# Kernel tuning notes

Hardware: AMD Instinct MI355X
Metric: run time of the kernel (lower is better)

## Reference

```python
import jax, jax.numpy as jnp
import numpy as np

B, N, H, E = 4, 256, 128, 16
EIN = 2 * H + 1 + E  # edge MLP input dim
LN_EPS = 1e-6  # flax nnx.LayerNorm default epsilon


def layer_norm(x, scale, bias):
    m = jnp.mean(x, axis=-1, keepdims=True)
    v = jnp.var(x, axis=-1, keepdims=True)
    return (x - m) * jax.lax.rsqrt(v + LN_EPS) * scale + bias


def mlp2(x, W1, b1, s, sb, W2, b2):
    # Linear -> LayerNorm -> ReLU -> Linear (dropout deterministic)
    h = jax.nn.relu(layer_norm(x @ W1 + b1, s, sb))
    return h @ W2 + b2


def setup_inputs() -> dict:
    key = jax.random.key(0)
    ks = jax.random.split(key, 24)

    def lin(k, fi, fo):
        k1, k2 = jax.random.split(k)
        W = jax.random.normal(k1, (fi, fo), jnp.float32) / np.sqrt(fi)
        b = jnp.zeros((fo,), jnp.float32)
        return W, b

    We1, be1 = lin(ks[0], EIN, H)
    We2, be2 = lin(ks[1], H, H)
    Wa, ba = lin(ks[2], EIN, 1)
    Wn1, bn1 = lin(ks[3], 2 * H, H)
    Wn2, bn2 = lin(ks[4], H, H)
    Wc1, bc1 = lin(ks[5], H, H)
    Wc2, bc2 = lin(ks[6], H, 1)

    return {
        "node_features": jax.random.normal(ks[7], (B, N, H), jnp.float32),
        "coordinates": jax.random.normal(ks[8], (B, N, 3), jnp.float32),
        "edge_features": jax.random.normal(ks[9], (B, N, N, E), jnp.float32),
        "mask": jnp.ones((B, N), jnp.float32),
        "We1": We1, "be1": be1,
        "ln_e_s": jnp.ones((H,), jnp.float32), "ln_e_b": jnp.zeros((H,), jnp.float32),
        "We2": We2, "be2": be2,
        "Wa": Wa, "ba": ba,
        "Wn1": Wn1, "bn1": bn1,
        "ln_n_s": jnp.ones((H,), jnp.float32), "ln_n_b": jnp.zeros((H,), jnp.float32),
        "Wn2": Wn2, "bn2": bn2,
        "Wc1": Wc1, "bc1": bc1,
        "ln_c_s": jnp.ones((H,), jnp.float32), "ln_c_b": jnp.zeros((H,), jnp.float32),
        "Wc2": Wc2, "bc2": bc2,
        "edge_index": jax.random.randint(ks[10], (B, N, N), 0, 2, jnp.int32),
    }


def reference(node_features, coordinates, edge_features, mask,
              We1, be1, ln_e_s, ln_e_b, We2, be2,
              Wa, ba,
              Wn1, bn1, ln_n_s, ln_n_b, Wn2, bn2,
              Wc1, bc1, ln_c_s, ln_c_b, Wc2, bc2,
              edge_index):
    b, n, h = node_features.shape
    rel_pos = coordinates[:, :, None, :] - coordinates[:, None, :, :]  # [B,N,N,3]
    d2 = jnp.sum(rel_pos ** 2, axis=-1, keepdims=True)                 # [B,N,N,1]

    node_i = jnp.broadcast_to(node_features[:, :, None, :], (b, n, n, h))
    node_j = jnp.broadcast_to(node_features[:, None, :, :], (b, n, n, h))
    edge_inputs = jnp.concatenate([node_i, node_j, d2, edge_features], axis=-1)  # [B,N,N,EIN]

    edge_messages = mlp2(edge_inputs, We1, be1, ln_e_s, ln_e_b, We2, be2)  # [B,N,N,H]
    new_edge_features = edge_messages

    att = jax.nn.sigmoid(edge_inputs @ Wa + ba)  # [B,N,N,1]
    adj = edge_index[..., None].astype(edge_messages.dtype)  # [B,N,N,1]
    msg_mask = (mask[:, :, None] * mask[:, None, :])[..., None]

    edge_messages = edge_messages * att * adj * msg_mask
    node_messages = jnp.sum(edge_messages, axis=2)  # [B,N,H]

    node_inputs = jnp.concatenate([node_features, node_messages], axis=-1)
    new_node_features = mlp2(node_inputs, Wn1, bn1, ln_n_s, ln_n_b, Wn2, bn2)

    coord_messages = mlp2(node_messages, Wc1, bc1, ln_c_s, ln_c_b, Wc2, bc2)  # [B,N,1]

    norm = jnp.sqrt(d2 + 1e-8)
    normalized_rel_pos = rel_pos / norm
    coord_update_dir = jnp.sum(normalized_rel_pos * att * adj, axis=2)  # [B,N,3]
    coord_updates = coord_update_dir * coord_messages * mask[:, :, None]
    new_coordinates = coordinates + coord_updates

    new_node_features = node_features + new_node_features  # residual
    return (new_node_features, new_coordinates, new_edge_features)
```

## Files before the change

### kernel.cpp

```cpp
#include <hip/hip_runtime.h>
#include <hip/hip_bf16.h>


typedef unsigned short ushort_t;
typedef __attribute__((ext_vector_type(8))) short short8;
typedef __attribute__((ext_vector_type(4))) float f32x4;

__device__ __forceinline__ ushort_t f2bf(float f) {
  unsigned int x = __builtin_bit_cast(unsigned int, f);
  x += 0x7fffu + ((x >> 16) & 1u);
  return (ushort_t)(x >> 16);
}

__global__ void k_sent777(float* out0) { out0[threadIdx.x] = 777.f; }

__global__ __launch_bounds__(128)
void k_pre(const float* nf, const float* We1, const float* be1,
           const float* Wa, float* pre_i, float* pre_j, float* api, float* apj) {
  int r = blockIdx.x, t = threadIdx.x;
  __shared__ float nfv[128];
  __shared__ float red[4];
  nfv[t] = nf[(size_t)r * 128 + t];
  __syncthreads();
  float s1 = be1[t], s2 = 0.f;
  for (int c = 0; c < 128; ++c) {
    float x = nfv[c];
    s1 += x * We1[c * 128 + t];
    s2 += x * We1[(128 + c) * 128 + t];
  }
  pre_i[(size_t)r * 128 + t] = s1;
  pre_j[(size_t)r * 128 + t] = s2;
  float t1 = nfv[t] * Wa[t];
  float t2 = nfv[t] * Wa[128 + t];
#pragma unroll
  for (int o = 32; o > 0; o >>= 1) { t1 += __shfl_down(t1, o); t2 += __shfl_down(t2, o); }
  if ((t & 63) == 0) { red[(t >> 6) * 2] = t1; red[(t >> 6) * 2 + 1] = t2; }
  __syncthreads();
  if (t == 0) { api[r] = red[0] + red[2]; apj[r] = red[1] + red[3]; }
}

__global__ __launch_bounds__(256)
void k_pack(const float* We2, ushort_t* bpack) {
  int t = blockIdx.x * 256 + threadIdx.x;
  if (t >= 2048) return;
  int ks = t >> 9, mt = (t >> 6) & 7, l = t & 63;
  int kb = ks * 32 + (l >> 4) * 8, col = mt * 16 + (l & 15);
#pragma unroll
  for (int e = 0; e < 8; ++e) bpack[t * 8 + e] = f2bf(We2[(kb + e) * 128 + col]);
}

__global__ __launch_bounds__(512, 4)
void k_edge(const float* co, const float* efo, const float* mk,
            const float* We1, const float* be2, const float* Wa, const float* ba,
            const float* lnes, const float* lneb, const int* eidx,
            const float* pre_i, const float* pre_j, const float* api, const float* apj,
            const ushort_t* bpack, float* oute, float* nm2, float* cd2) {
  __shared__ __align__(16) ushort_t h1s[128 * 136];
  __shared__ float wef[17 * 128];
  __shared__ float lns[128], lnb[128];
  __shared__ float attw[128];
  __shared__ float lnS[512], lnSS[512];
  __shared__ float nmp[8][128];
  __shared__ float cred[2][3];

  const int bx = blockIdx.x;
  const int r = bx >> 1, half = bx & 1;
  const int b = r >> 8;
  const int t = threadIdx.x;
  const int lane = t & 63, w = t >> 6;

  for (int q = t; q < 17 * 128; q += 512) {
    int e = q >> 7, c = q & 127;
    int row = (e < 16) ? (257 + e) : 256;
    wef[q] = We1[row * 128 + c];
  }
  if (t < 128) { lns[t] = lnes[t]; }
  else if (t < 256) { lnb[t - 128] = lneb[t - 128]; }
  __syncthreads();

  const int jr = t & 127, ch = t >> 7;
  const int j = half * 128 + jr;
  const int gj = b * 256 + j;

  float dx = co[r * 3 + 0] - co[gj * 3 + 0];
  float dy = co[r * 3 + 1] - co[gj * 3 + 1];
  float dz = co[r * 3 + 2] - co[gj * 3 + 2];
  float d2 = dx * dx + dy * dy + dz * dz;

  float efv[17];
  {
    const float* efp = efo + ((size_t)r * 256 + j) * 16;
    f32x4 e0 = *reinterpret_cast<const f32x4*>(efp);
    f32x4 e1 = *reinterpret_cast<const f32x4*>(efp + 4);
    f32x4 e2 = *reinterpret_cast<const f32x4*>(efp + 8);
    f32x4 e3 = *reinterpret_cast<const f32x4*>(efp + 12);
#pragma unroll
    for (int x = 0; x < 4; ++x) {
      efv[x] = e0[x]; efv[4 + x] = e1[x]; efv[8 + x] = e2[x]; efv[12 + x] = e3[x];
    }
  }
  efv[16] = d2;

  if (ch == 0) {
    float a = api[r] + apj[gj] + ba[0] + d2 * Wa[256];
#pragma unroll
    for (int e = 0; e < 16; ++e) a += efv[e] * Wa[257 + e];
    float att = 1.f / (1.f + __expf(-a));
    float aw = att * (float)eidx[(size_t)r * 256 + j];
    attw[jr] = aw * mk[r] * mk[gj];
    float invn = rsqrtf(d2 + 1e-8f);
    float c0 = dx * invn * aw, c1 = dy * invn * aw, c2 = dz * invn * aw;
#pragma unroll
    for (int o = 32; o > 0; o >>= 1) {
      c0 += __shfl_down(c0, o); c1 += __shfl_down(c1, o); c2 += __shfl_down(c2, o);
    }
    if (lane == 0) { cred[w][0] = c0; cred[w][1] = c1; cred[w][2] = c2; }
  }

  const int cbase = ch * 32;
  const f32x4* pi4 = reinterpret_cast<const f32x4*>(pre_i + (size_t)r * 128 + cbase);
  const f32x4* pj4 = reinterpret_cast<const f32x4*>(pre_j + (size_t)gj * 128 + cbase);
  const f32x4* wef4 = reinterpret_cast<const f32x4*>(wef);
  float h[32];
  float s = 0.f, ss = 0.f;
#pragma unroll
  for (int c4 = 0; c4 < 8; ++c4) {
    f32x4 v = pi4[c4] + pj4[c4];
#pragma unroll
    for (int e = 0; e < 17; ++e) v += efv[e] * wef4[e * 32 + (cbase >> 2) + c4];
#pragma unroll
    for (int x = 0; x < 4; ++x) { h[c4 * 4 + x] = v[x]; s += v[x]; ss += v[x] * v[x]; }
  }
  lnS[t] = s; lnSS[t] = ss;
  __syncthreads();
  float st  = lnS[jr] + lnS[jr + 128] + lnS[jr + 256] + lnS[jr + 384];
  float sst = lnSS[jr] + lnSS[jr + 128] + lnSS[jr + 256] + lnSS[jr + 384];
  float mean = st * (1.f / 128.f);
  float var = fmaxf(sst * (1.f / 128.f) - mean * mean, 0.f);
  float rsv = rsqrtf(var + 1e-6f);
  ushort_t* hrow = h1s + jr * 136 + cbase;
#pragma unroll
  for (int q8 = 0; q8 < 4; ++q8) {
    short8 pk;
#pragma unroll
    for (int x = 0; x < 8; ++x) {
      int c = q8 * 8 + x;
      float gv = (h[c] - mean) * rsv * lns[cbase + c] + lnb[cbase + c];
      pk[x] = (short)f2bf(fmaxf(gv, 0.f));
    }
    *reinterpret_cast<short8*>(hrow + q8 * 8) = pk;
  }
  __syncthreads();

  if (t == 0) {
#pragma unroll
    for (int d = 0; d < 3; ++d)
      cd2[(size_t)(half * 1024 + r) * 3 + d] = cred[0][d] + cred[1][d];
  }

  f32x4 acc[8];
#pragma unroll
  for (int mt = 0; mt < 8; ++mt) acc[mt] = (f32x4){0.f, 0.f, 0.f, 0.f};

  const short* h1p = reinterpret_cast<const short*>(h1s);
  const int nrow = w * 16 + (lane & 15);
#pragma unroll
  for (int ks = 0; ks < 4; ++ks) {
    short8 hfr = *reinterpret_cast<const short8*>(
        h1p + nrow * 136 + ks * 32 + ((lane >> 4) * 8));
#pragma unroll
    for (int mt = 0; mt < 8; ++mt) {
      short8 afr = *reinterpret_cast<const short8*>(bpack + (((ks * 8 + mt) * 64 + lane) * 8));
      acc[mt] = __builtin_amdgcn_mfma_f32_16x16x32_bf16(afr, hfr, acc[mt], 0, 0, 0);
    }
  }

  const size_t obase = ((size_t)r * 256 + half * 128) * 128;
  const float wgt = attw[nrow];
  const int mq = (lane >> 4) * 4;
  float pm[8][4];
#pragma unroll
  for (int mt = 0; mt < 8; ++mt) {
    f32x4 b4 = *reinterpret_cast<const f32x4*>(be2 + mt * 16 + mq);
    f32x4 val = acc[mt] + b4;
    *reinterpret_cast<f32x4*>(oute + obase + (size_t)nrow * 128 + mt * 16 + mq) = val;
#pragma unroll
    for (int x = 0; x < 4; ++x) pm[mt][x] = val[x] * wgt;
  }
#pragma unroll
  for (int mt = 0; mt < 8; ++mt)
#pragma unroll
    for (int x = 0; x < 4; ++x) {
      float v = pm[mt][x];
      v += __shfl_xor(v, 1); v += __shfl_xor(v, 2);
      v += __shfl_xor(v, 4); v += __shfl_xor(v, 8);
      pm[mt][x] = v;
    }
  if ((lane & 15) == 0) {
#pragma unroll
    for (int mt = 0; mt < 8; ++mt)
#pragma unroll
      for (int x = 0; x < 4; ++x) nmp[w][mt * 16 + mq + x] = pm[mt][x];
  }
  __syncthreads();
  if (t < 128) {
    float acc8 = nmp[0][t] + nmp[1][t] + nmp[2][t] + nmp[3][t]
               + nmp[4][t] + nmp[5][t] + nmp[6][t] + nmp[7][t];
    nm2[(size_t)(half * 1024 + r) * 128 + t] = acc8;
  }
}

__device__ __forceinline__ float bsum128(float v, float* red, int t) {
#pragma unroll
  for (int o = 32; o > 0; o >>= 1) v += __shfl_down(v, o);
  __syncthreads();
  if ((t & 63) == 0) red[t >> 6] = v;
  __syncthreads();
  return red[0] + red[1];
}

__global__ __launch_bounds__(128)
void k_node(const float* nf, const float* co, const float* mk,
            const float* Wn1, const float* bn1, const float* lnns, const float* lnnb,
            const float* Wn2, const float* bn2,
            const float* Wc1, const float* bc1, const float* lncs, const float* lncb,
            const float* Wc2, const float* bc2,
            const float* nm2, const float* cd2,
            float* out0, float* out1) {
  int r = blockIdx.x, t = threadIdx.x;
  __shared__ float nin[256];
  __shared__ float hf[128];
  __shared__ float red[2];
  float nfv = nf[(size_t)r * 128 + t];
  float nmv = nm2[(size_t)r * 128 + t] + nm2[(size_t)(1024 + r) * 128 + t];
  nin[t] = nfv; nin[128 + t] = nmv;
  __syncthreads();
  float s1 = bn1[t];
  for (int c = 0; c < 256; ++c) s1 += nin[c] * Wn1[c * 128 + t];
  float mean = bsum128(s1, red, t) * (1.f / 128.f);
  float var = fmaxf(bsum128(s1 * s1, red, t) * (1.f / 128.f) - mean * mean, 0.f);
  float hv = (s1 - mean) * rsqrtf(var + 1e-6f) * lnns[t] + lnnb[t];
  hv = fmaxf(hv, 0.f);
  hf[t] = hv;
  __syncthreads();
  float o1 = bn2[t] + nfv;
  for (int c = 0; c < 128; ++c) o1 += hf[c] * Wn2[c * 128 + t];
  out0[(size_t)r * 128 + t] = o1;
  float g = bc1[t];
  for (int c = 0; c < 128; ++c) g += nin[128 + c] * Wc1[c * 128 + t];
  float gm = bsum128(g, red, t) * (1.f / 128.f);
  float gv = fmaxf(bsum128(g * g, red, t) * (1.f / 128.f) - gm * gm, 0.f);
  float gh = fmaxf((g - gm) * rsqrtf(gv + 1e-6f) * lncs[t] + lncb[t], 0.f);
  float cm = bsum128(gh * Wc2[t], red, t) + bc2[0];
  if (t < 3) {
    float cd = cd2[(size_t)r * 3 + t] + cd2[(size_t)(1024 + r) * 3 + t];
    float nc = co[(size_t)r * 3 + t] + cd * cm * mk[r];
    out1[(size_t)r * 3 + t] = nc;
  }
}

extern "C" void kernel_launch(void* const* d_in, const int* in_sizes, int n_in,
                              void* d_out, int out_size, void* d_ws, size_t ws_size,
                              hipStream_t stream) {
  const float* nf   = (const float*)d_in[0];
  const float* co   = (const float*)d_in[1];
  const float* efo  = (const float*)d_in[2];
  const float* mk   = (const float*)d_in[3];
  const float* We1  = (const float*)d_in[4];
  const float* be1  = (const float*)d_in[5];
  const float* lnes = (const float*)d_in[6];
  const float* lneb = (const float*)d_in[7];
  const float* We2  = (const float*)d_in[8];
  const float* be2  = (const float*)d_in[9];
  const float* Wa   = (const float*)d_in[10];
  const float* ba   = (const float*)d_in[11];
  const float* Wn1  = (const float*)d_in[12];
  const float* bn1  = (const float*)d_in[13];
  const float* lnns = (const float*)d_in[14];
  const float* lnnb = (const float*)d_in[15];
  const float* Wn2  = (const float*)d_in[16];
  const float* bn2  = (const float*)d_in[17];
  const float* Wc1  = (const float*)d_in[18];
  const float* bc1  = (const float*)d_in[19];
  const float* lncs = (const float*)d_in[20];
  const float* lncb = (const float*)d_in[21];
  const float* Wc2  = (const float*)d_in[22];
  const float* bc2  = (const float*)d_in[23];
  const int* eidx   = (const int*)d_in[24];

  float* out0 = (float*)d_out;
  float* out1 = out0 + 131072;
  float* oute = out1 + 3072;

  const size_t need = (size_t)(131072 + 131072 + 1024 + 1024 + 262144 + 6144) * 4 + 16384 * 2;
  if (ws_size < need) {
    k_sent777<<<1, 128, 0, stream>>>(out0);
    return;
  }
  float* ws    = (float*)d_ws;
  float* pre_i = ws;
  float* pre_j = pre_i + 131072;
  float* api   = pre_j + 131072;
  float* apj   = api + 1024;
  float* nm2   = apj + 1024;
  float* cd2   = nm2 + 262144;
  ushort_t* bpack = (ushort_t*)(cd2 + 6144);

  k_pre<<<1024, 128, 0, stream>>>(nf, We1, be1, Wa, pre_i, pre_j, api, apj);
  k_pack<<<8, 256, 0, stream>>>(We2, bpack);
  k_edge<<<2048, 512, 0, stream>>>(co, efo, mk, We1, be2, Wa, ba, lnes, lneb, eidx,
                                   pre_i, pre_j, api, apj, bpack, oute, nm2, cd2);
  k_node<<<1024, 128, 0, stream>>>(nf, co, mk, Wn1, bn1, lnns, lnnb, Wn2, bn2,
                                   Wc1, bc1, lncs, lncb, Wc2, bc2, nm2, cd2, out0, out1);
}
```

Baseline: 114.3 us.

## Compute first edge-MLP layer's edge-feature projection with bf16 MFMA

Replaces the per-thread scalar FMA loop over 17 edge inputs with a bf16 MFMA 16x16x32 call. The A operand (edge features plus d2, zero-padded) is staged in LDS and the We1 fragment is held in registers. LayerNorm statistics are now computed from a bf16-rounded copy of the hidden row written to LDS, and the old partial-sum arrays and weight LDS tables are removed. Occupancy hint is lowered from 4 to 2 blocks per CU. This adds bf16 rounding of the edge features and pre-LN values, which may hurt accuracy, plus extra LDS passes and uncoalesced per-element h1s writes.

```diff
diff --git a/kernel.cpp b/kernel.cpp
--- a/kernel.cpp
+++ b/kernel.cpp
@@ -10,6 +10,10 @@
   unsigned int x = __builtin_bit_cast(unsigned int, f);
   x += 0x7fffu + ((x >> 16) & 1u);
   return (ushort_t)(x >> 16);
+}
+__device__ __forceinline__ float bf2f(ushort_t u) {
+  unsigned int x = ((unsigned int)u) << 16;
+  return __builtin_bit_cast(float, x);
 }
 
 __global__ void k_sent777(float* out0) { out0[threadIdx.x] = 777.f; }
@@ -49,17 +53,16 @@
   for (int e = 0; e < 8; ++e) bpack[t * 8 + e] = f2bf(We2[(kb + e) * 128 + col]);
 }
 
-__global__ __launch_bounds__(512, 4)
+__global__ __launch_bounds__(512, 2)
 void k_edge(const float* co, const float* efo, const float* mk,
             const float* We1, const float* be2, const float* Wa, const float* ba,
             const float* lnes, const float* lneb, const int* eidx,
             const float* pre_i, const float* pre_j, const float* api, const float* apj,
             const ushort_t* bpack, float* oute, float* nm2, float* cd2) {
+  __shared__ __align__(16) ushort_t A_lds[8 * 64 * 8];
   __shared__ __align__(16) ushort_t h1s[128 * 136];
-  __shared__ float wef[17 * 128];
-  __shared__ float lns[128], lnb[128];
+  __shared__ float2 mrsv[128];
   __shared__ float attw[128];
-  __shared__ float lnS[512], lnSS[512];
   __shared__ float nmp[8][128];
   __shared__ float cred[2][3];
 
@@ -68,27 +71,47 @@
   const int b = r >> 8;
   const int t = threadIdx.x;
   const int lane = t & 63, w = t >> 6;
-
-  for (int q = t; q < 17 * 128; q += 512) {
-    int e = q >> 7, c = q & 127;
-    int row = (e < 16) ? (257 + e) : 256;
-    wef[q] = We1[row * 128 + c];
-  }
-  if (t < 128) { lns[t] = lnes[t]; }
-  else if (t < 256) { lnb[t - 128] = lneb[t - 128]; }
-  __syncthreads();
-
-  const int jr = t & 127, ch = t >> 7;
-  const int j = half * 128 + jr;
-  const int gj = b * 256 + j;
-
-  float dx = co[r * 3 + 0] - co[gj * 3 + 0];
-  float dy = co[r * 3 + 1] - co[gj * 3 + 1];
-  float dz = co[r * 3 + 2] - co[gj * 3 + 2];
-  float d2 = dx * dx + dy * dy + dz * dz;
-
-  float efv[17];
+  const int s4 = lane >> 4;
+  const int chan = w * 16 + (lane & 15);
+  const int gbase = b * 256 + half * 128;
+
+  short8 wfrag;
+#pragma unroll
+  for (int e = 0; e < 8; ++e) {
+    int k = s4 * 8 + e;
+    float wv = 0.f;
+    if (k < 16) wv = We1[(257 + k) * 128 + chan];
+    else if (k == 16) wv = We1[256 * 128 + chan];
+    wfrag[e] = (short)f2bf(wv);
+  }
+  const float preIc = pre_i[(size_t)r * 128 + chan];
+  const float lnsc = lnes[chan], lnbc = lneb[chan];
+
   {
+    const int mt = t >> 6, l = t & 63, sl = l >> 4, row = mt * 16 + (l & 15);
+    short8* dst = reinterpret_cast<short8*>(A_lds + ((size_t)(mt * 64 + l)) * 8);
+    if (sl < 2) {
+      const float* efp = efo + ((size_t)(r * 256 + half * 128 + row)) * 16 + sl * 8;
+      f32x4 e0 = *reinterpret_cast<const f32x4*>(efp);
+      f32x4 e1 = *reinterpret_cast<const f32x4*>(efp + 4);
+      short8 pk;
+#pragma unroll
+      for (int x = 0; x < 4; ++x) { pk[x] = (short)f2bf(e0[x]); pk[4 + x] = (short)f2bf(e1[x]); }
+      *dst = pk;
+    } else if (sl == 3) {
+      *dst = (short8){0, 0, 0, 0, 0, 0, 0, 0};
+    }
+  }
+
+  if (t < 128) {
+    const int j = half * 128 + t;
+    const int gj = b * 256 + j;
+    float dx = co[r * 3 + 0] - co[gj * 3 + 0];
+    float dy = co[r * 3 + 1] - co[gj * 3 + 1];
+    float dz = co[r * 3 + 2] - co[gj * 3 + 2];
+    float d2 = dx * dx + dy * dy + dz * dz;
+
+    float a = api[r] + apj[gj] + ba[0] + d2 * Wa[256];
     const float* efp = efo + ((size_t)r * 256 + j) * 16;
     f32x4 e0 = *reinterpret_cast<const f32x4*>(efp);
     f32x4 e1 = *reinterpret_cast<const f32x4*>(efp + 4);
@@ -96,18 +119,17 @@
     f32x4 e3 = *reinterpret_cast<const f32x4*>(efp + 12);
 #pragma unroll
     for (int x = 0; x < 4; ++x) {
-      efv[x] = e0[x]; efv[4 + x] = e1[x]; efv[8 + x] = e2[x]; efv[12 + x] = e3[x];
-    }
-  }
-  efv[16] = d2;
-
-  if (ch == 0) {
-    float a = api[r] + apj[gj] + ba[0] + d2 * Wa[256];
-#pragma unroll
-    for (int e = 0; e < 16; ++e) a += efv[e] * Wa[257 + e];
+      a += e0[x] * Wa[257 + x] + e1[x] * Wa[261 + x]
+         + e2[x] * Wa[265 + x] + e3[x] * Wa[269 + x];
+    }
     float att = 1.f / (1.f + __expf(-a));
     float aw = att * (float)eidx[(size_t)r * 256 + j];
-    attw[jr] = aw * mk[r] * mk[gj];
+    attw[t] = aw * mk[r] * mk[gj];
+
+    short8 dz8 = (short8){0, 0, 0, 0, 0, 0, 0, 0};
+    dz8[0] = (short)f2bf(d2);
+    *reinterpret_cast<short8*>(A_lds + ((size_t)((t >> 4) * 64 + 32 + (t & 15))) * 8) = dz8;
+
     float invn = rsqrtf(d2 + 1e-8f);
     float c0 = dx * invn * aw, c1 = dy * invn * aw, c2 = dz * invn * aw;
 #pragma unroll
@@ -116,39 +138,54 @@
     }
     if (lane == 0) { cred[w][0] = c0; cred[w][1] = c1; cred[w][2] = c2; }
   }
-
-  const int cbase = ch * 32;
-  const f32x4* pi4 = reinterpret_cast<const f32x4*>(pre_i + (size_t)r * 128 + cbase);
-  const f32x4* pj4 = reinterpret_cast<const f32x4*>(pre_j + (size_t)gj * 128 + cbase);
-  const f32x4* wef4 = reinterpret_cast<const f32x4*>(wef);
-  float h[32];
-  float s = 0.f, ss = 0.f;
-#pragma unroll
-  for (int c4 = 0; c4 < 8; ++c4) {
-    f32x4 v = pi4[c4] + pj4[c4];
-#pragma unroll
-    for (int e = 0; e < 17; ++e) v += efv[e] * wef4[e * 32 + (cbase >> 2) + c4];
-#pragma unroll
-    for (int x = 0; x < 4; ++x) { h[c4 * 4 + x] = v[x]; s += v[x]; ss += v[x] * v[x]; }
-  }
-  lnS[t] = s; lnSS[t] = ss;
-  __syncthreads();
-  float st  = lnS[jr] + lnS[jr + 128] + lnS[jr + 256] + lnS[jr + 384];
-  float sst = lnSS[jr] + lnSS[jr + 128] + lnSS[jr + 256] + lnSS[jr + 384];
-  float mean = st * (1.f / 128.f);
-  float var = fmaxf(sst * (1.f / 128.f) - mean * mean, 0.f);
-  float rsv = rsqrtf(var + 1e-6f);
-  ushort_t* hrow = h1s + jr * 136 + cbase;
-#pragma unroll
-  for (int q8 = 0; q8 < 4; ++q8) {
-    short8 pk;
-#pragma unroll
-    for (int x = 0; x < 8; ++x) {
-      int c = q8 * 8 + x;
-      float gv = (h[c] - mean) * rsv * lns[cbase + c] + lnb[cbase + c];
-      pk[x] = (short)f2bf(fmaxf(gv, 0.f));
-    }
-    *reinterpret_cast<short8*>(hrow + q8 * 8) = pk;
+  __syncthreads();
+
+  f32x4 acc1[8];
+#pragma unroll
+  for (int mt = 0; mt < 8; ++mt) {
+    short8 afr = *reinterpret_cast<const short8*>(A_lds + ((size_t)(mt * 64 + lane)) * 8);
+    acc1[mt] = __builtin_amdgcn_mfma_f32_16x16x32_bf16(
+        afr, wfrag, (f32x4){0.f, 0.f, 0.f, 0.f}, 0, 0, 0);
+  }
+#pragma unroll
+  for (int mt = 0; mt < 8; ++mt) {
+#pragma unroll
+    for (int reg = 0; reg < 4; ++reg) {
+      int row = mt * 16 + s4 * 4 + reg;
+      float v = acc1[mt][reg] + preIc + pre_j[((size_t)(gbase + row)) * 128 + chan];
+      acc1[mt][reg] = v;
+      h1s[row * 136 + chan] = f2bf(v);
+    }
+  }
+  __syncthreads();
+
+  if (t < 128) {
+    const short8* hr8 = reinterpret_cast<const short8*>(h1s + t * 136);
+    float sum = 0.f, ss = 0.f;
+#pragma unroll
+    for (int q = 0; q < 16; ++q) {
+      short8 pk = hr8[q];
+#pragma unroll
+      for (int x = 0; x < 8; ++x) {
+        float f = bf2f((ushort_t)pk[x]);
+        sum += f; ss += f * f;
+      }
+    }
+    float mean = sum * (1.f / 128.f);
+    float var = fmaxf(ss * (1.f / 128.f) - mean * mean, 0.f);
+    mrsv[t] = make_float2(mean, rsqrtf(var + 1e-6f));
+  }
+  __syncthreads();
+
+#pragma unroll
+  for (int mt = 0; mt < 8; ++mt) {
+#pragma unroll
+    for (int reg = 0; reg < 4; ++reg) {
+      int row = mt * 16 + s4 * 4 + reg;
+      float2 mr = mrsv[row];
+      float gv = (acc1[mt][reg] - mr.x) * mr.y * lnsc + lnbc;
+      h1s[row * 136 + chan] = f2bf(fmaxf(gv, 0.f));
+    }
   }
   __syncthreads();
 
@@ -167,7 +204,7 @@
 #pragma unroll
   for (int ks = 0; ks < 4; ++ks) {
     short8 hfr = *reinterpret_cast<const short8*>(
-        h1p + nrow * 136 + ks * 32 + ((lane >> 4) * 8));
+        h1p + nrow * 136 + ks * 32 + (s4 * 8));
 #pragma unroll
     for (int mt = 0; mt < 8; ++mt) {
       short8 afr = *reinterpret_cast<const short8*>(bpack + (((ks * 8 + mt) * 64 + lane) * 8));
@@ -177,7 +214,7 @@
 
   const size_t obase = ((size_t)r * 256 + half * 128) * 128;
   const float wgt = attw[nrow];
-  const int mq = (lane >> 4) * 4;
+  const int mq = s4 * 4;
   float pm[8][4];
 #pragma unroll
   for (int mt = 0; mt < 8; ++mt) {
```

Result: faster. 101.1 us (-11.5%).

## Compute edge first-layer features with MFMA and per-wave LayerNorm reductions

Applied to the files above, without the earlier changes.

The fp32 FMA loop over the 17 edge-feature and distance inputs is replaced by a bf16 MFMA against a prepacked We1 slice, and each wave now owns 16 edge rows in the MFMA layout. LayerNorm statistics are reduced with cross-lane shuffles instead of shared-memory staging, which removes the weight and LN-parameter shared buffers and one barrier. Attention and coordinate reductions are done per wave with xor shuffles. Launch bounds are raised to 8 waves/SIMD occupancy hint. The cost is bf16 rounding of edge features and d2 in the first layer, which could hurt accuracy.

```diff
diff --git a/kernel.cpp b/kernel.cpp
--- a/kernel.cpp
+++ b/kernel.cpp
@@ -4,6 +4,7 @@
 
 typedef unsigned short ushort_t;
 typedef __attribute__((ext_vector_type(8))) short short8;
+typedef __attribute__((ext_vector_type(4))) short short4_t;
 typedef __attribute__((ext_vector_type(4))) float f32x4;
 
 __device__ __forceinline__ ushort_t f2bf(float f) {
@@ -40,46 +41,47 @@
 }
 
 __global__ __launch_bounds__(256)
-void k_pack(const float* We2, ushort_t* bpack) {
+void k_pack(const float* We2, const float* We1, ushort_t* bpack, ushort_t* wpack) {
   int t = blockIdx.x * 256 + threadIdx.x;
-  if (t >= 2048) return;
-  int ks = t >> 9, mt = (t >> 6) & 7, l = t & 63;
-  int kb = ks * 32 + (l >> 4) * 8, col = mt * 16 + (l & 15);
-#pragma unroll
-  for (int e = 0; e < 8; ++e) bpack[t * 8 + e] = f2bf(We2[(kb + e) * 128 + col]);
-}
-
-__global__ __launch_bounds__(512, 4)
+  if (t < 2048) {
+    int ks = t >> 9, mt = (t >> 6) & 7, l = t & 63;
+    int kb = ks * 32 + (l >> 4) * 8, col = mt * 16 + (l & 15);
+#pragma unroll
+    for (int e = 0; e < 8; ++e) bpack[t * 8 + e] = f2bf(We2[(kb + e) * 128 + col]);
+  } else if (t < 2560) {
+    int q = t - 2048;
+    int mt = q >> 6, l = q & 63;
+    int chan = mt * 16 + (l & 15), kb = (l >> 4) * 8;
+#pragma unroll
+    for (int e = 0; e < 8; ++e) {
+      int k = kb + e;
+      float wv = 0.f;
+      if (k < 16) wv = We1[(257 + k) * 128 + chan];
+      else if (k == 16) wv = We1[256 * 128 + chan];
+      wpack[q * 8 + e] = f2bf(wv);
+    }
+  }
+}
+
+__global__ __launch_bounds__(512, 8)
 void k_edge(const float* co, const float* efo, const float* mk,
-            const float* We1, const float* be2, const float* Wa, const float* ba,
+            const float* be2, const float* Wa, const float* ba,
             const float* lnes, const float* lneb, const int* eidx,
             const float* pre_i, const float* pre_j, const float* api, const float* apj,
-            const ushort_t* bpack, float* oute, float* nm2, float* cd2) {
+            const ushort_t* bpack, const ushort_t* wpack,
+            float* oute, float* nm2, float* cd2) {
   __shared__ __align__(16) ushort_t h1s[128 * 136];
-  __shared__ float wef[17 * 128];
-  __shared__ float lns[128], lnb[128];
-  __shared__ float attw[128];
-  __shared__ float lnS[512], lnSS[512];
   __shared__ float nmp[8][128];
-  __shared__ float cred[2][3];
+  __shared__ float cred[8][3];
 
   const int bx = blockIdx.x;
   const int r = bx >> 1, half = bx & 1;
   const int b = r >> 8;
   const int t = threadIdx.x;
   const int lane = t & 63, w = t >> 6;
-
-  for (int q = t; q < 17 * 128; q += 512) {
-    int e = q >> 7, c = q & 127;
-    int row = (e < 16) ? (257 + e) : 256;
-    wef[q] = We1[row * 128 + c];
-  }
-  if (t < 128) { lns[t] = lnes[t]; }
-  else if (t < 256) { lnb[t - 128] = lneb[t - 128]; }
-  __syncthreads();
-
-  const int jr = t & 127, ch = t >> 7;
-  const int j = half * 128 + jr;
+  const int s4 = lane >> 4, li = lane & 15;
+  const int row = w * 16 + li;
+  const int j = half * 128 + row;
   const int gj = b * 256 + j;
 
   float dx = co[r * 3 + 0] - co[gj * 3 + 0];
@@ -87,75 +89,87 @@
   float dz = co[r * 3 + 2] - co[gj * 3 + 2];
   float d2 = dx * dx + dy * dy + dz * dz;
 
-  float efv[17];
+  short8 bfr = (short8){0, 0, 0, 0, 0, 0, 0, 0};
+  float dot = 0.f;
+  if (s4 < 2) {
+    const float* efp = efo + ((size_t)r * 256 + j) * 16 + s4 * 8;
+    f32x4 a0 = *reinterpret_cast<const f32x4*>(efp);
+    f32x4 a1 = *reinterpret_cast<const f32x4*>(efp + 4);
+#pragma unroll
+    for (int x = 0; x < 4; ++x) { bfr[x] = (short)f2bf(a0[x]); bfr[4 + x] = (short)f2bf(a1[x]); }
+    const float* wap = Wa + 257 + s4 * 8;
+#pragma unroll
+    for (int x = 0; x < 4; ++x) dot += a0[x] * wap[x] + a1[x] * wap[4 + x];
+  } else if (s4 == 2) {
+    bfr[0] = (short)f2bf(d2);
+    dot = api[r] + apj[gj] + ba[0] + d2 * Wa[256];
+  }
+  dot += __shfl_xor(dot, 16);
+  dot += __shfl_xor(dot, 32);
+  float att = 1.f / (1.f + __expf(-dot));
+  float aw = att * (float)eidx[(size_t)r * 256 + j];
+  const float wgt = aw * mk[r] * mk[gj];
+
   {
-    const float* efp = efo + ((size_t)r * 256 + j) * 16;
-    f32x4 e0 = *reinterpret_cast<const f32x4*>(efp);
-    f32x4 e1 = *reinterpret_cast<const f32x4*>(efp + 4);
-    f32x4 e2 = *reinterpret_cast<const f32x4*>(efp + 8);
-    f32x4 e3 = *reinterpret_cast<const f32x4*>(efp + 12);
+    float invn = rsqrtf(d2 + 1e-8f);
+    float c0 = (s4 == 0) ? dx * invn * aw : 0.f;
+    float c1 = (s4 == 0) ? dy * invn * aw : 0.f;
+    float c2 = (s4 == 0) ? dz * invn * aw : 0.f;
+#pragma unroll
+    for (int o = 1; o < 64; o <<= 1) {
+      c0 += __shfl_xor(c0, o); c1 += __shfl_xor(c1, o); c2 += __shfl_xor(c2, o);
+    }
+    if (lane == 0) { cred[w][0] = c0; cred[w][1] = c1; cred[w][2] = c2; }
+  }
+
+  f32x4 acc1[8];
+#pragma unroll
+  for (int mt = 0; mt < 8; ++mt) {
+    short8 wfr = *reinterpret_cast<const short8*>(wpack + ((size_t)(mt * 64 + lane)) * 8);
+    acc1[mt] = __builtin_amdgcn_mfma_f32_16x16x32_bf16(
+        wfr, bfr, (f32x4){0.f, 0.f, 0.f, 0.f}, 0, 0, 0);
+  }
+
+  const float* pir = pre_i + (size_t)r * 128;
+  const float* pjr = pre_j + (size_t)gj * 128;
+  float s = 0.f, ss = 0.f;
+#pragma unroll
+  for (int mt = 0; mt < 8; ++mt) {
+    const int c0i = mt * 16 + s4 * 4;
+    f32x4 pj = *reinterpret_cast<const f32x4*>(pjr + c0i);
+    f32x4 pi = *reinterpret_cast<const f32x4*>(pir + c0i);
+    acc1[mt] += pi + pj;
+#pragma unroll
+    for (int x = 0; x < 4; ++x) { s += acc1[mt][x]; ss += acc1[mt][x] * acc1[mt][x]; }
+  }
+  s += __shfl_xor(s, 16);  s += __shfl_xor(s, 32);
+  ss += __shfl_xor(ss, 16); ss += __shfl_xor(ss, 32);
+  const float mean = s * (1.f / 128.f);
+  const float var = fmaxf(ss * (1.f / 128.f) - mean * mean, 0.f);
+  const float rsv = rsqrtf(var + 1e-6f);
+
+  ushort_t* hrow = h1s + row * 136;
+#pragma unroll
+  for (int mt = 0; mt < 8; ++mt) {
+    const int c0i = mt * 16 + s4 * 4;
+    f32x4 ln4 = *reinterpret_cast<const f32x4*>(lnes + c0i);
+    f32x4 lb4 = *reinterpret_cast<const f32x4*>(lneb + c0i);
+    short4_t pk;
 #pragma unroll
     for (int x = 0; x < 4; ++x) {
-      efv[x] = e0[x]; efv[4 + x] = e1[x]; efv[8 + x] = e2[x]; efv[12 + x] = e3[x];
-    }
-  }
-  efv[16] = d2;
-
-  if (ch == 0) {
-    float a = api[r] + apj[gj] + ba[0] + d2 * Wa[256];
-#pragma unroll
-    for (int e = 0; e < 16; ++e) a += efv[e] * Wa[257 + e];
-    float att = 1.f / (1.f + __expf(-a));
-    float aw = att * (float)eidx[(size_t)r * 256 + j];
-    attw[jr] = aw * mk[r] * mk[gj];
-    float invn = rsqrtf(d2 + 1e-8f);
-    float c0 = dx * invn * aw, c1 = dy * invn * aw, c2 = dz * invn * aw;
-#pragma unroll
-    for (int o = 32; o > 0; o >>= 1) {
-      c0 += __shfl_down(c0, o); c1 += __shfl_down(c1, o); c2 += __shfl_down(c2, o);
-    }
-    if (lane == 0) { cred[w][0] = c0; cred[w][1] = c1; cred[w][2] = c2; }
-  }
-
-  const int cbase = ch * 32;
-  const f32x4* pi4 = reinterpret_cast<const f32x4*>(pre_i + (size_t)r * 128 + cbase);
-  const f32x4* pj4 = reinterpret_cast<const f32x4*>(pre_j + (size_t)gj * 128 + cbase);
-  const f32x4* wef4 = reinterpret_cast<const f32x4*>(wef);
-  float h[32];
-  float s = 0.f, ss = 0.f;
-#pragma unroll
-  for (int c4 = 0; c4 < 8; ++c4) {
-    f32x4 v = pi4[c4] + pj4[c4];
-#pragma unroll
-    for (int e = 0; e < 17; ++e) v += efv[e] * wef4[e * 32 + (cbase >> 2) + c4];
-#pragma unroll
-    for (int x = 0; x < 4; ++x) { h[c4 * 4 + x] = v[x]; s += v[x]; ss += v[x] * v[x]; }
-  }
-  lnS[t] = s; lnSS[t] = ss;
-  __syncthreads();
-  float st  = lnS[jr] + lnS[jr + 128] + lnS[jr + 256] + lnS[jr + 384];
-  float sst = lnSS[jr] + lnSS[jr + 128] + lnSS[jr + 256] + lnSS[jr + 384];
-  float mean = st * (1.f / 128.f);
-  float var = fmaxf(sst * (1.f / 128.f) - mean * mean, 0.f);
-  float rsv = rsqrtf(var + 1e-6f);
-  ushort_t* hrow = h1s + jr * 136 + cbase;
-#pragma unroll
-  for (int q8 = 0; q8 < 4; ++q8) {
-    short8 pk;
-#pragma unroll
-    for (int x = 0; x < 8; ++x) {
-      int c = q8 * 8 + x;
-      float gv = (h[c] - mean) * rsv * lns[cbase + c] + lnb[cbase + c];
+      float gv = (acc1[mt][x] - mean) * rsv * ln4[x] + lb4[x];
       pk[x] = (short)f2bf(fmaxf(gv, 0.f));
     }
-    *reinterpret_cast<short8*>(hrow + q8 * 8) = pk;
+    *reinterpret_cast<short4_t*>(hrow + c0i) = pk;
   }
   __syncthreads();
 
   if (t == 0) {
 #pragma unroll
     for (int d = 0; d < 3; ++d)
-      cd2[(size_t)(half * 1024 + r) * 3 + d] = cred[0][d] + cred[1][d];
+      cd2[(size_t)(half * 1024 + r) * 3 + d] =
+          ((cred[0][d] + cred[1][d]) + (cred[2][d] + cred[3][d]))
+        + ((cred[4][d] + cred[5][d]) + (cred[6][d] + cred[7][d]));
   }
 
   f32x4 acc[8];
@@ -163,11 +177,9 @@
   for (int mt = 0; mt < 8; ++mt) acc[mt] = (f32x4){0.f, 0.f, 0.f, 0.f};
 
   const short* h1p = reinterpret_cast<const short*>(h1s);
-  const int nrow = w * 16 + (lane & 15);
 #pragma unroll
   for (int ks = 0; ks < 4; ++ks) {
-    short8 hfr = *reinterpret_cast<const short8*>(
-        h1p + nrow * 136 + ks * 32 + ((lane >> 4) * 8));
+    short8 hfr = *reinterpret_cast<const short8*>(h1p + row * 136 + ks * 32 + s4 * 8);
 #pragma unroll
     for (int mt = 0; mt < 8; ++mt) {
       short8 afr = *reinterpret_cast<const short8*>(bpack + (((ks * 8 + mt) * 64 + lane) * 8));
@@ -176,14 +188,13 @@
   }
 
   const size_t obase = ((size_t)r * 256 + half * 128) * 128;
-  const float wgt = attw[nrow];
-  const int mq = (lane >> 4) * 4;
+  const int mq = s4 * 4;
   float pm[8][4];
 #pragma unroll
   for (int mt = 0; mt < 8; ++mt) {
     f32x4 b4 = *reinterpret_cast<const f32x4*>(be2 + mt * 16 + mq);
     f32x4 val = acc[mt] + b4;
-    *reinterpret_cast<f32x4*>(oute + obase + (size_t)nrow * 128 + mt * 16 + mq) = val;
+    *reinterpret_cast<f32x4*>(oute + obase + (size_t)row * 128 + mt * 16 + mq) = val;
 #pragma unroll
     for (int x = 0; x < 4; ++x) pm[mt][x] = val[x] * wgt;
   }
@@ -196,7 +207,7 @@
       v += __shfl_xor(v, 4); v += __shfl_xor(v, 8);
       pm[mt][x] = v;
     }
-  if ((lane & 15) == 0) {
+  if (li == 0) {
 #pragma unroll
     for (int mt = 0; mt < 8; ++mt)
 #pragma unroll
@@ -204,8 +215,8 @@
   }
   __syncthreads();
   if (t < 128) {
-    float acc8 = nmp[0][t] + nmp[1][t] + nmp[2][t] + nmp[3][t]
-               + nmp[4][t] + nmp[5][t] + nmp[6][t] + nmp[7][t];
+    float acc8 = ((nmp[0][t] + nmp[1][t]) + (nmp[2][t] + nmp[3][t]))
+               + ((nmp[4][t] + nmp[5][t]) + (nmp[6][t] + nmp[7][t]));
     nm2[(size_t)(half * 1024 + r) * 128 + t] = acc8;
   }
 }
@@ -292,7 +303,8 @@
   float* out1 = out0 + 131072;
   float* oute = out1 + 3072;
 
-  const size_t need = (size_t)(131072 + 131072 + 1024 + 1024 + 262144 + 6144) * 4 + 16384 * 2;
+  const size_t need = (size_t)(131072 + 131072 + 1024 + 1024 + 262144 + 6144) * 4
+                    + (16384 + 4096) * 2;
   if (ws_size < need) {
     k_sent777<<<1, 128, 0, stream>>>(out0);
     return;
@@ -305,11 +317,13 @@
   float* nm2   = apj + 1024;
   float* cd2   = nm2 + 262144;
   ushort_t* bpack = (ushort_t*)(cd2 + 6144);
+  ushort_t* wpack = bpack + 16384;
 
   k_pre<<<1024, 128, 0, stream>>>(nf, We1, be1, Wa, pre_i, pre_j, api, apj);
-  k_pack<<<8, 256, 0, stream>>>(We2, bpack);
-  k_edge<<<2048, 512, 0, stream>>>(co, efo, mk, We1, be2, Wa, ba, lnes, lneb, eidx,
-                                   pre_i, pre_j, api, apj, bpack, oute, nm2, cd2);
+  k_pack<<<10, 256, 0, stream>>>(We2, We1, bpack, wpack);
+  k_edge<<<2048, 512, 0, stream>>>(co, efo, mk, be2, Wa, ba, lnes, lneb, eidx,
+                                   pre_i, pre_j, api, apj, bpack, wpack,
+                                   oute, nm2, cd2);
   k_node<<<1024, 128, 0, stream>>>(nf, co, mk, Wn1, bn1, lnns, lnnb, Wn2, bn2,
                                    Wc1, bc1, lncs, lncb, Wc2, bc2, nm2, cd2, out0, out1);
 }
```

New measurement: 115.1 us. Within noise of the previous version (+0.7%).
